# Kernel optimization log

Measured on AMD Instinct MI355X. Metric: run time of the kernel, lower is better.

The kernel has to match this reference:

```python
import jax, jax.numpy as jnp
import numpy as np

B, S, E, H = 2, 2048, 1024, 16
DH = E // H


def setup_inputs() -> dict:
    key = jax.random.key(0)
    ks = jax.random.split(key, 12)
    std = 1.0 / np.sqrt(E)
    inp = {
        "query": jax.random.normal(ks[0], (B, S, E), jnp.float32),
        "key": jax.random.normal(ks[1], (B, S, E), jnp.float32),
        "value": jax.random.normal(ks[2], (B, S, E), jnp.float32),
        "mask": jax.random.randint(ks[3], (B, 1, 1, S), 0, 2, jnp.int32),
        "Wq": jax.random.normal(ks[4], (E, E), jnp.float32) * std,
        "bq": jnp.zeros((E,), jnp.float32),
        "Wk": jax.random.normal(ks[5], (E, E), jnp.float32) * std,
        "bk": jnp.zeros((E,), jnp.float32),
        "Wv": jax.random.normal(ks[6], (E, E), jnp.float32) * std,
        "bv": jnp.zeros((E,), jnp.float32),
        "Wo": jax.random.normal(ks[7], (E, E), jnp.float32) * std,
        "bo": jnp.zeros((E,), jnp.float32),
    }
    return inp


def reference(query, key, value, mask, Wq, bq, Wk, bk, Wv, bv, Wo, bo):
    b = query.shape[0]
    # QKV projections, then split heads: [B,S,E] -> [B,H,S,Dh]
    def split_heads(x):
        return x.reshape(b, -1, H, DH).transpose(0, 2, 1, 3)
    q = split_heads(query @ Wq + bq)
    k = split_heads(key @ Wk + bk)
    v = split_heads(value @ Wv + bv)
    # explicit bmm -> mask -> softmax -> bmm (non-SDPA), scores [B,H,Sq,Sk]
    scores = jnp.einsum("bhqd,bhkd->bhqk", q, k) / np.sqrt(DH).astype(np.float32)
    scores = jnp.where(mask == 0, jnp.float32(-1e9), scores)
    attn = jax.nn.softmax(scores, axis=-1)  # dropout is identity in eval mode
    out = jnp.einsum("bhqk,bhkd->bhqd", attn, v)
    out = out.transpose(0, 2, 1, 3).reshape(b, -1, E)  # merge heads
    return out @ Wo + bo
```

## Files before the change

### kernel.cpp

```cpp
#include <hip/hip_runtime.h>
#include <hip/hip_bf16.h>
#include <stdint.h>

#define B_ 2
#define S_ 2048
#define E_ 1024
#define H_ 16
#define DH_ 64
#define MELEMS (4096 * 1024)
#define WE (1024 * 1024)

typedef unsigned short u16;
typedef __bf16 bf16x8 __attribute__((ext_vector_type(8)));
typedef u16 u16x8 __attribute__((ext_vector_type(8)));
typedef u16 u16x4 __attribute__((ext_vector_type(4)));
typedef float f32x4 __attribute__((ext_vector_type(4)));
typedef float f32x16 __attribute__((ext_vector_type(16)));
typedef uint32_t u32x4 __attribute__((ext_vector_type(4)));
typedef uint32_t u32x2v __attribute__((ext_vector_type(2)));

__device__ __forceinline__ float bf2f(u16 u) {
    union { uint32_t i; float f; } v; v.i = ((uint32_t)u) << 16; return v.f;
}
__device__ __forceinline__ u16 f2bf(float f) {
    union { float f; uint32_t i; } v; v.f = f;
    uint32_t r = (v.i + 0x7FFFu + ((v.i >> 16) & 1u)) >> 16;
    return (u16)r;
}
__device__ __forceinline__ uint32_t cvtpk(float a, float b) {
    uint32_t r;
    asm("v_cvt_pk_bf16_f32 %0, %1, %2" : "=v"(r) : "v"(a), "v"(b));
    return r;
}
__device__ __forceinline__ bf16x8 ldfrag(const u16* p) {
    u16x8 t = *(const u16x8*)p;
    return __builtin_bit_cast(bf16x8, t);
}
__device__ __forceinline__ void gld16(const void* g, void* l) {
    __builtin_amdgcn_global_load_lds(
        (const __attribute__((address_space(1))) void*)g,
        (__attribute__((address_space(3))) void*)l, 16, 0, 0);
}

__global__ __launch_bounds__(256)
void cvt_all(const float* __restrict__ q, const float* __restrict__ k,
             const float* __restrict__ v,
             const float* __restrict__ W0, const float* __restrict__ W1,
             const float* __restrict__ W2, const float* __restrict__ W3,
             u16* __restrict__ Qi, u16* __restrict__ Ki, u16* __restrict__ Vi,
             u16* __restrict__ T0, u16* __restrict__ T1,
             u16* __restrict__ T2, u16* __restrict__ T3)
{
    __shared__ float tile[64][65];
    const int bid = blockIdx.x;
    const int tid = threadIdx.x;

    if (bid < 6144) {
        const int z = bid >> 11;
        const int cx = bid & 2047;
        const float* src = (z == 0) ? q : (z == 1) ? k : v;
        u16* dst = (z == 0) ? Qi : (z == 1) ? Ki : Vi;
        const size_t i8 = ((size_t)cx * 256 + tid) * 8;
        float4 f0 = *(const float4*)&src[i8];
        float4 f1 = *(const float4*)&src[i8 + 4];
        u16x8 t;
        t[0] = f2bf(f0.x); t[1] = f2bf(f0.y); t[2] = f2bf(f0.z); t[3] = f2bf(f0.w);
        t[4] = f2bf(f1.x); t[5] = f2bf(f1.y); t[6] = f2bf(f1.z); t[7] = f2bf(f1.w);
        *(u16x8*)&dst[i8] = t;
    } else {
        const int rr = bid - 6144;
        const int z = rr >> 8;
        const int tt = rr & 255;
        const float* W = (z == 0) ? W0 : (z == 1) ? W1 : (z == 2) ? W2 : W3;
        u16* T = (z == 0) ? T0 : (z == 1) ? T1 : (z == 2) ? T2 : T3;
        const int n0 = (tt & 15) * 64, k0 = (tt >> 4) * 64;
        const int r = tid >> 2, c0 = (tid & 3) * 16;

        #pragma unroll
        for (int i = 0; i < 4; ++i) {
            float4 w = *(const float4*)&W[(size_t)(k0 + r) * 1024 + n0 + c0 + i * 4];
            tile[r][c0 + i * 4 + 0] = w.x; tile[r][c0 + i * 4 + 1] = w.y;
            tile[r][c0 + i * 4 + 2] = w.z; tile[r][c0 + i * 4 + 3] = w.w;
        }
        __syncthreads();
        u16x8 a, b;
        #pragma unroll
        for (int j = 0; j < 8; ++j) a[j] = f2bf(tile[c0 + j][r]);
        #pragma unroll
        for (int j = 0; j < 8; ++j) b[j] = f2bf(tile[c0 + 8 + j][r]);
        *(u16x8*)&T[(size_t)(n0 + r) * 1024 + k0 + c0] = a;
        *(u16x8*)&T[(size_t)(n0 + r) * 1024 + k0 + c0 + 8] = b;
    }
}

template<int BN>
__global__ __launch_bounds__(256)
void gemm_bt(const u16* __restrict__ A0, const u16* __restrict__ A1,
             const u16* __restrict__ A2,
             const u16* __restrict__ Bt0, const u16* __restrict__ Bt1,
             const u16* __restrict__ Bt2,
             const float* __restrict__ b0, const float* __restrict__ b1,
             const float* __restrict__ b2,
             void* __restrict__ C0, void* __restrict__ C1, void* __restrict__ C2,
             const int* __restrict__ mask,
             int c_f32, int vt_z, float scale0, int K)
{
    const int z = blockIdx.z;
    const u16* A  = (z == 0) ? A0 : (z == 1) ? A1 : A2;
    const u16* Bt = (z == 0) ? Bt0 : (z == 1) ? Bt1 : Bt2;
    const float* bias = (z == 0) ? b0 : (z == 1) ? b1 : b2;
    void* C = (z == 0) ? C0 : (z == 1) ? C1 : C2;
    const float scale = (z == 0) ? scale0 : 1.0f;

    __shared__ alignas(16) u16 As[128 * 32];
    __shared__ alignas(16) u16 Bs[BN * 32];

    const int tid  = threadIdx.x;
    const int lane = tid & 63;
    const int wv   = tid >> 6;
    const int l15  = lane & 15;
    const int quad = lane >> 4;
    const int m0 = blockIdx.y * 128;
    const int n0 = blockIdx.x * BN;
    const int wr = (wv >> 1) * 64;
    const int wc = (wv & 1) * (BN / 2);

    const int srow = wv * 16 + (lane >> 2);
    const int skk  = (lane & 3) * 8;

    constexpr int NJ = BN / 32;
    f32x4 acc[4][NJ] = {};

    for (int k0 = 0; k0 < K; k0 += 32) {
        __syncthreads();
        #pragma unroll
        for (int h = 0; h < 2; ++h) {
            const int r = h * 64 + srow;
            gld16(&A[(size_t)(m0 + r) * K + k0 + skk], &As[r * 32 + skk]);
        }
        #pragma unroll
        for (int h = 0; h < BN / 64; ++h) {
            const int r = h * 64 + srow;
            gld16(&Bt[(size_t)(n0 + r) * K + k0 + skk], &Bs[r * 32 + skk]);
        }
        __syncthreads();

        bf16x8 a[4], b[NJ];
        #pragma unroll
        for (int i = 0; i < 4; ++i)
            a[i] = ldfrag(&As[(wr + i * 16 + l15) * 32 + quad * 8]);
        #pragma unroll
        for (int j = 0; j < NJ; ++j)
            b[j] = ldfrag(&Bs[(wc + j * 16 + l15) * 32 + quad * 8]);
        #pragma unroll
        for (int i = 0; i < 4; ++i)
            #pragma unroll
            for (int j = 0; j < NJ; ++j)
                acc[i][j] = __builtin_amdgcn_mfma_f32_16x16x32_bf16(
                    a[i], b[j], acc[i][j], 0, 0, 0);
    }

    #pragma unroll
    for (int j = 0; j < NJ; ++j) {
        const int col = n0 + wc + j * 16 + l15;
        const float bcol = bias[col];
        #pragma unroll
        for (int i = 0; i < 4; ++i) {
            const int row0 = m0 + wr + i * 16 + quad * 4;
            if (z == vt_z) {
                const int bb = row0 >> 11, s0 = row0 & 2047;
                const int4 mv = *(const int4*)&mask[bb * S_ + s0];
                u16x4 t;
                t[0] = mv.x ? f2bf((acc[i][j][0] + bcol) * scale) : (u16)0;
                t[1] = mv.y ? f2bf((acc[i][j][1] + bcol) * scale) : (u16)0;
                t[2] = mv.z ? f2bf((acc[i][j][2] + bcol) * scale) : (u16)0;
                t[3] = mv.w ? f2bf((acc[i][j][3] + bcol) * scale) : (u16)0;
                *(u16x4*)&((u16*)C)[((size_t)bb * E_ + col) * S_ + s0] = t;
            } else {
                #pragma unroll
                for (int r = 0; r < 4; ++r) {
                    const int row = row0 + r;
                    const float v = (acc[i][j][r] + bcol) * scale;
                    if (c_f32) ((float*)C)[(size_t)row * 1024 + col] = v;
                    else       ((u16*)C)[(size_t)row * 1024 + col]  = f2bf(v);
                }
            }
        }
    }
}

__global__ __launch_bounds__(512, 4)
void attn_v12(const u16* __restrict__ Q, const u16* __restrict__ K,
              const u16* __restrict__ Vt_g, const int* __restrict__ mask,
              u16* __restrict__ ctx)
{
    __shared__ alignas(16) u16 smem[2][8192];
    __shared__ alignas(16) u16 Mbf[S_];
    __shared__ float scrl[256];

    const int tid  = threadIdx.x;
    const int lane = tid & 63;
    const int wv   = tid >> 6;
    const int l31  = lane & 31;
    const int half = lane >> 5;
    const int sw7  = lane & 7;
    const int qw   = wv & 3;
    const int kh   = wv >> 2;
    const int kbase = kh * 32;
    const int qt = blockIdx.x;
    const int bh = blockIdx.y;
    const int b  = bh >> 4, h = bh & 15;

    const size_t qk_off = (size_t)b * S_ * E_ + (size_t)h * DH_;
    const size_t vt_off = ((size_t)b * E_ + (size_t)h * DH_) * S_;
    const int* mrow = &mask[b * S_];

    {
        const int i = tid * 4;
        const int4 m = *(const int4*)&mrow[i];
        u16x4 t;
        t[0] = m.x ? (u16)0x3F80 : (u16)0;
        t[1] = m.y ? (u16)0x3F80 : (u16)0;
        t[2] = m.z ? (u16)0x3F80 : (u16)0;
        t[3] = m.w ? (u16)0x3F80 : (u16)0;
        *(u16x4*)&Mbf[i] = t;
    }

    const int q0 = qt * 128 + qw * 32;
    bf16x8 qf[4];
    #pragma unroll
    for (int s = 0; s < 4; ++s)
        qf[s] = ldfrag(&Q[qk_off + (size_t)(q0 + l31) * E_ + s * 16 + half * 8]);

    f32x16 O[2] = {};
    f32x16 lacc = {};

    auto stage = [&](int kc, int buf) {
        const int rr = tid >> 3;
        const int ks = tid & 7;
        const int gb = ks ^ (rr & 7);
        gld16(&K[qk_off + (size_t)(kc + rr) * E_ + gb * 8],
              &smem[buf][rr * 64 + ks * 8]);
        gld16(&Vt_g[vt_off + (size_t)rr * S_ + kc + gb * 8],
              &smem[buf][4096 + rr * 64 + ks * 8]);
    };

    stage(0, 0);
    int cur = 0;

    for (int kc = 0; kc < S_; kc += 64) {
        __syncthreads();
        if (kc + 64 < S_) stage(kc + 64, cur ^ 1);
        const u16* Kb = &smem[cur][0];
        const u16* Vb = &smem[cur][4096];

        __builtin_amdgcn_s_setprio(1);
        f32x16 St = {};
        #pragma unroll
        for (int s = 0; s < 4; ++s) {
            bf16x8 kf = ldfrag(&Kb[(kbase + l31) * 64 + ((s * 2 + half) ^ sw7) * 8]);
            St = __builtin_amdgcn_mfma_f32_32x32x16_bf16(kf, qf[s], St, 0, 0, 0);
        }
        __builtin_amdgcn_s_setprio(0);
        float ex[16];
        #pragma unroll
        for (int i = 0; i < 16; ++i) ex[i] = __builtin_exp2f(St[i]);

        uint32_t wd[8];
        #pragma unroll
        for (int i = 0; i < 8; ++i) wd[i] = cvtpk(ex[2 * i], ex[2 * i + 1]);

        u32x2v r02 = __builtin_amdgcn_permlane32_swap(wd[0], wd[2], false, false);
        u32x2v r13 = __builtin_amdgcn_permlane32_swap(wd[1], wd[3], false, false);
        u32x2v r46 = __builtin_amdgcn_permlane32_swap(wd[4], wd[6], false, false);
        u32x2v r57 = __builtin_amdgcn_permlane32_swap(wd[5], wd[7], false, false);
        u32x4 f0, f1;
        f0[0] = r02[0]; f0[1] = r13[0]; f0[2] = r02[1]; f0[3] = r13[1];
        f1[0] = r46[0]; f1[1] = r57[0]; f1[2] = r46[1]; f1[3] = r57[1];
        const bf16x8 pa0 = __builtin_bit_cast(bf16x8, f0);
        const bf16x8 pa1 = __builtin_bit_cast(bf16x8, f1);

        __builtin_amdgcn_s_setprio(1);
        {
            bf16x8 mb0 = ldfrag(&Mbf[kc + kbase + half * 8]);
            bf16x8 mb1 = ldfrag(&Mbf[kc + kbase + 16 + half * 8]);
            lacc = __builtin_amdgcn_mfma_f32_32x32x16_bf16(pa0, mb0, lacc, 0, 0, 0);
            lacc = __builtin_amdgcn_mfma_f32_32x32x16_bf16(pa1, mb1, lacc, 0, 0, 0);
        }

        #pragma unroll
        for (int nt = 0; nt < 2; ++nt) {
            const int drow = nt * 32 + l31;
            const int kb0 = kh * 4 + half;
            const int kb1 = kh * 4 + 2 + half;
            bf16x8 vb0 = ldfrag(&Vb[drow * 64 + (kb0 ^ sw7) * 8]);
            bf16x8 vb1 = ldfrag(&Vb[drow * 64 + (kb1 ^ sw7) * 8]);
            O[nt] = __builtin_amdgcn_mfma_f32_32x32x16_bf16(pa0, vb0, O[nt], 0, 0, 0);
            O[nt] = __builtin_amdgcn_mfma_f32_32x32x16_bf16(pa1, vb1, O[nt], 0, 0, 0);
        }
        __builtin_amdgcn_s_setprio(0);
        cur ^= 1;
    }

    __syncthreads();
    float* scr = (float*)smem;
    const int sbase = (qw * 64 + lane) * 32;
    if (kh == 1) {
        #pragma unroll
        for (int j = 0; j < 4; ++j) {
            f32x4 t0, t1;
            #pragma unroll
            for (int r = 0; r < 4; ++r) { t0[r] = O[0][j * 4 + r]; t1[r] = O[1][j * 4 + r]; }
            *(f32x4*)&scr[sbase + (j ^ sw7) * 4]       = t0;
            *(f32x4*)&scr[sbase + ((j + 4) ^ sw7) * 4] = t1;
        }
        if (l31 == 0) {
            #pragma unroll
            for (int i = 0; i < 16; ++i)
                scrl[qw * 32 + half * 16 + i] = lacc[i];
        }
    }
    __syncthreads();
    if (kh == 0) {
        #pragma unroll
        for (int nt = 0; nt < 2; ++nt) {
            #pragma unroll
            for (int j = 0; j < 4; ++j) {
                const f32x4 p = *(const f32x4*)&scr[sbase + (((nt * 4 + j) ^ sw7)) * 4];
                #pragma unroll
                for (int r = 0; r < 4; ++r) {
                    const int i  = j * 4 + r;
                    const int ql = (i & 3) + 8 * (i >> 2) + 4 * half;
                    const float lt = lacc[i] + scrl[qw * 32 + half * 16 + i];
                    const float o  = O[nt][i] + p[r];
                    const int q = q0 + ql;
                    const int e = h * DH_ + nt * 32 + l31;
                    ctx[((size_t)b * S_ + q) * E_ + e] = f2bf(o / lt);
                }
            }
        }
    }
}

__global__ __launch_bounds__(256)
void gemm_bias(const void* __restrict__ A, int a_f32,
               const float* __restrict__ W, const float* __restrict__ bias,
               void* __restrict__ C, int c_f32,
               int M, int N, int K, float scale)
{
    __shared__ alignas(16) u16 As[64 * 32];
    __shared__ alignas(16) u16 Wt[64 * 32];
    const int tid  = threadIdx.x;
    const int lane = tid & 63;
    const int wv   = tid >> 6;
    const int l15  = lane & 15;
    const int quad = lane >> 4;
    const int m0 = blockIdx.y * 64, n0 = blockIdx.x * 64;
    const int wr = (wv >> 1) * 32, wc = (wv & 1) * 32;
    const int ar = tid >> 2, ac = (tid & 3) * 8;
    const int wk = tid >> 3, wn = (tid & 7) * 8;
    f32x4 acc[2][2] = {};
    for (int k0 = 0; k0 < K; k0 += 32) {
        __syncthreads();
        if (a_f32) {
            const float* Af = (const float*)A;
            const float* p = &Af[(size_t)(m0 + ar) * K + k0 + ac];
            float4 f0 = *(const float4*)p; float4 f1 = *(const float4*)(p + 4);
            u16x8 t;
            t[0] = f2bf(f0.x); t[1] = f2bf(f0.y); t[2] = f2bf(f0.z); t[3] = f2bf(f0.w);
            t[4] = f2bf(f1.x); t[5] = f2bf(f1.y); t[6] = f2bf(f1.z); t[7] = f2bf(f1.w);
            *(u16x8*)&As[ar * 32 + ac] = t;
        } else {
            const u16* Ab = (const u16*)A;
            *(u16x8*)&As[ar * 32 + ac] = *(const u16x8*)&Ab[(size_t)(m0 + ar) * K + k0 + ac];
        }
        {
            const float* p = &W[(size_t)(k0 + wk) * N + n0 + wn];
            float4 g0 = *(const float4*)p; float4 g1 = *(const float4*)(p + 4);
            float fv[8] = {g0.x, g0.y, g0.z, g0.w, g1.x, g1.y, g1.z, g1.w};
            #pragma unroll
            for (int j = 0; j < 8; ++j) Wt[(wn + j) * 32 + wk] = f2bf(fv[j]);
        }
        __syncthreads();
        bf16x8 a[2], b[2];
        #pragma unroll
        for (int sm = 0; sm < 2; ++sm) a[sm] = ldfrag(&As[(wr + sm * 16 + l15) * 32 + quad * 8]);
        #pragma unroll
        for (int sn = 0; sn < 2; ++sn) b[sn] = ldfrag(&Wt[(wc + sn * 16 + l15) * 32 + quad * 8]);
        #pragma unroll
        for (int sm = 0; sm < 2; ++sm)
            #pragma unroll
            for (int sn = 0; sn < 2; ++sn)
                acc[sm][sn] = __builtin_amdgcn_mfma_f32_16x16x32_bf16(a[sm], b[sn], acc[sm][sn], 0, 0, 0);
    }
    #pragma unroll
    for (int sm = 0; sm < 2; ++sm)
        #pragma unroll
        for (int sn = 0; sn < 2; ++sn) {
            const int col = n0 + wc + sn * 16 + l15;
            const float bcol = bias[col];
            #pragma unroll
            for (int r = 0; r < 4; ++r) {
                const int row = m0 + wr + sm * 16 + quad * 4 + r;
                const float v = (acc[sm][sn][r] + bcol) * scale;
                if (c_f32) ((float*)C)[(size_t)row * N + col] = v;
                else       ((u16*)C)[(size_t)row * N + col]  = f2bf(v);
            }
        }
}

__global__ __launch_bounds__(256)
void attn_v2(const u16* __restrict__ Q, const u16* __restrict__ K,
             const u16* __restrict__ V, const int* __restrict__ mask,
             u16* __restrict__ ctx, int BH_per_B)
{
    __shared__ alignas(16) u16 Ks[64 * 72];
    __shared__ alignas(16) u16 Vt[64 * 72];
    __shared__ alignas(16) u16 Pb[4][16 * 72];
    const int tid  = threadIdx.x;
    const int lane = tid & 63;
    const int wv   = tid >> 6;
    const int l15  = lane & 15;
    const int quad = lane >> 4;
    const int qt = blockIdx.x;
    const int bh = blockIdx.y;
    const int b  = bh / BH_per_B, h = bh % BH_per_B;
    const size_t headoff = (size_t)b * S_ * E_ + (size_t)h * DH_;
    const int qrow = qt * 64 + wv * 16 + l15;
    const bf16x8 qf0 = ldfrag(&Q[headoff + (size_t)qrow * E_ + quad * 8]);
    const bf16x8 qf1 = ldfrag(&Q[headoff + (size_t)qrow * E_ + 32 + quad * 8]);
    f32x4 oacc[4] = {};
    float mrun[4] = {-1e30f, -1e30f, -1e30f, -1e30f};
    float lrun[4] = {0.f, 0.f, 0.f, 0.f};
    const int skey = tid >> 2;
    const int sd0  = (tid & 3) * 16;
    for (int kc = 0; kc < S_; kc += 64) {
        __syncthreads();
        {
            const u16* kg = &K[headoff + (size_t)(kc + skey) * E_ + sd0];
            *(u16x8*)&Ks[skey * 72 + sd0]     = *(const u16x8*)kg;
            *(u16x8*)&Ks[skey * 72 + sd0 + 8] = *(const u16x8*)(kg + 8);
            const u16* vg = &V[headoff + (size_t)(kc + skey) * E_ + sd0];
            u16x8 v0 = *(const u16x8*)vg;
            u16x8 v1 = *(const u16x8*)(vg + 8);
            #pragma unroll
            for (int j = 0; j < 8; ++j) {
                const int d = sd0 + j;
                Vt[d * 72 + (skey ^ (((d >> 3) & 7) * 8))] = v0[j];
            }
            #pragma unroll
            for (int j = 0; j < 8; ++j) {
                const int d = sd0 + 8 + j;
                Vt[d * 72 + (skey ^ (((d >> 3) & 7) * 8))] = v1[j];
            }
        }
        __syncthreads();
        f32x4 sb[4];
        #pragma unroll
        for (int t = 0; t < 4; ++t) {
            bf16x8 kf0 = ldfrag(&Ks[(t * 16 + l15) * 72 + quad * 8]);
            bf16x8 kf1 = ldfrag(&Ks[(t * 16 + l15) * 72 + 32 + quad * 8]);
            f32x4 s = {};
            s = __builtin_amdgcn_mfma_f32_16x16x32_bf16(qf0, kf0, s, 0, 0, 0);
            s = __builtin_amdgcn_mfma_f32_16x16x32_bf16(qf1, kf1, s, 0, 0, 0);
            const int mv = mask[b * S_ + kc + t * 16 + l15];
            #pragma unroll
            for (int r = 0; r < 4; ++r) sb[t][r] = (mv == 0) ? -1e9f : s[r];
        }
        #pragma unroll
        for (int r = 0; r < 4; ++r) {
            float m = fmaxf(fmaxf(sb[0][r], sb[1][r]), fmaxf(sb[2][r], sb[3][r]));
            #pragma unroll
            for (int off = 1; off < 16; off <<= 1) m = fmaxf(m, __shfl_xor(m, off));
            const float mnew  = fmaxf(mrun[r], m);
            const float alpha = __expf(mrun[r] - mnew);
            mrun[r] = mnew;
            float sum = 0.f;
            #pragma unroll
            for (int t = 0; t < 4; ++t) {
                const float p = __expf(sb[t][r] - mnew);
                sb[t][r] = p; sum += p;
            }
            #pragma unroll
            for (int off = 1; off < 16; off <<= 1) sum += __shfl_xor(sum, off);
            lrun[r] = lrun[r] * alpha + sum;
            #pragma unroll
            for (int c = 0; c < 4; ++c) oacc[c][r] *= alpha;
        }
        #pragma unroll
        for (int t = 0; t < 4; ++t)
            #pragma unroll
            for (int r = 0; r < 4; ++r)
                Pb[wv][(quad * 4 + r) * 72 + t * 16 + l15] = f2bf(sb[t][r]);
        const bf16x8 pa0 = ldfrag(&Pb[wv][l15 * 72 + quad * 8]);
        const bf16x8 pa1 = ldfrag(&Pb[wv][l15 * 72 + 32 + quad * 8]);
        #pragma unroll
        for (int c = 0; c < 4; ++c) {
            const int d = c * 16 + l15;
            const int sg = ((d >> 3) & 7) * 8;
            bf16x8 vb0 = ldfrag(&Vt[d * 72 + ((quad * 8) ^ sg)]);
            bf16x8 vb1 = ldfrag(&Vt[d * 72 + ((32 + quad * 8) ^ sg)]);
            oacc[c] = __builtin_amdgcn_mfma_f32_16x16x32_bf16(pa0, vb0, oacc[c], 0, 0, 0);
            oacc[c] = __builtin_amdgcn_mfma_f32_16x16x32_bf16(pa1, vb1, oacc[c], 0, 0, 0);
        }
    }
    #pragma unroll
    for (int c = 0; c < 4; ++c) {
        const int e = h * DH_ + c * 16 + l15;
        #pragma unroll
        for (int r = 0; r < 4; ++r) {
            const int qg = qt * 64 + wv * 16 + quad * 4 + r;
            ctx[((size_t)b * S_ + qg) * E_ + e] = f2bf(oacc[c][r] / lrun[r]);
        }
    }
}

extern "C" void kernel_launch(void* const* d_in, const int* in_sizes, int n_in,
                              void* d_out, int out_size, void* d_ws, size_t ws_size,
                              hipStream_t stream)
{
    const float* query = (const float*)d_in[0];
    const float* key   = (const float*)d_in[1];
    const float* value = (const float*)d_in[2];
    const int*   mask  = (const int*)d_in[3];
    const float* Wq = (const float*)d_in[4];  const float* bq = (const float*)d_in[5];
    const float* Wk = (const float*)d_in[6];  const float* bk = (const float*)d_in[7];
    const float* Wv = (const float*)d_in[8];  const float* bv = (const float*)d_in[9];
    const float* Wo = (const float*)d_in[10]; const float* bo = (const float*)d_in[11];
    float* out = (float*)d_out;

    u16* ws = (u16*)d_ws;
    dim3 blk(256);

    const size_t need_fancy = (size_t)(6 * MELEMS + 4 * WE) * sizeof(u16);
    const size_t need_full  = (size_t)(4 * MELEMS) * sizeof(u16) + 64;

    if (ws_size >= need_fancy) {
        u16* Qi  = ws;
        u16* Ki  = Qi + MELEMS;
        u16* Vi  = Ki + MELEMS;
        u16* Wqt = Vi + MELEMS;
        u16* Wkt = Wqt + WE;
        u16* Wvt = Wkt + WE;
        u16* Wot = Wvt + WE;
        u16* Qp  = Wot + WE;
        u16* Kp  = Qp + MELEMS;
        u16* Vp  = Kp + MELEMS;
        u16* Cp  = Qi;

        cvt_all<<<dim3(7168), blk, 0, stream>>>(query, key, value,
                                                Wq, Wk, Wv, Wo,
                                                Qi, Ki, Vi, Wqt, Wkt, Wvt, Wot);

        gemm_bt<128><<<dim3(8, 32, 3), blk, 0, stream>>>(
            Qi, Ki, Vi, Wqt, Wkt, Wvt, bq, bk, bv,
            Qp, Kp, Vp, mask, 0, 2, 0.125f * 1.44269504f, E_);

        attn_v12<<<dim3(S_ / 128, B_ * H_), dim3(512), 0, stream>>>(
            Qp, Kp, Vp, mask, Cp);

        gemm_bt<64><<<dim3(16, 32, 1), blk, 0, stream>>>(
            Cp, Cp, Cp, Wot, Wot, Wot, bo, bo, bo,
            out, out, out, mask, 1, -1, 1.0f, E_);
    } else if (ws_size >= need_full) {
        u16* Qp = ws;
        u16* Kp = ws + MELEMS;
        u16* Vp = ws + 2 * MELEMS;
        u16* Cp = ws + 3 * MELEMS;
        const int M = B_ * S_;
        dim3 gg(E_ / 64, M / 64);
        gemm_bias<<<gg, blk, 0, stream>>>(query, 1, Wq, bq, Qp, 0, M, E_, E_, 0.125f);
        gemm_bias<<<gg, blk, 0, stream>>>(key,   1, Wk, bk, Kp, 0, M, E_, E_, 1.0f);
        gemm_bias<<<gg, blk, 0, stream>>>(value, 1, Wv, bv, Vp, 0, M, E_, E_, 1.0f);
        attn_v2<<<dim3(S_ / 64, B_ * H_), blk, 0, stream>>>(Qp, Kp, Vp, mask, Cp, H_);
        gemm_bias<<<gg, blk, 0, stream>>>(Cp, 0, Wo, bo, out, 1, M, E_, E_, 1.0f);
    } else {
        const size_t szb = (size_t)S_ * E_;
        u16* Qp = ws; u16* Kp = ws + szb; u16* Vp = ws + 2 * szb; u16* Cp = ws + 3 * szb;
        dim3 gg(E_ / 64, S_ / 64);
        for (int b = 0; b < B_; ++b) {
            gemm_bias<<<gg, blk, 0, stream>>>(query + b * szb, 1, Wq, bq, Qp, 0, S_, E_, E_, 0.125f);
            gemm_bias<<<gg, blk, 0, stream>>>(key   + b * szb, 1, Wk, bk, Kp, 0, S_, E_, E_, 1.0f);
            gemm_bias<<<gg, blk, 0, stream>>>(value + b * szb, 1, Wv, bv, Vp, 0, S_, E_, E_, 1.0f);
            attn_v2<<<dim3(S_ / 64, H_), blk, 0, stream>>>(Qp, Kp, Vp, mask + b * S_, Cp, H_);
            gemm_bias<<<gg, blk, 0, stream>>>(Cp, 0, Wo, bo, ((float*)d_out) + b * szb, 1, S_, E_, E_, 1.0f);
        }
    }
}
```

Before: 149.8 us.

## Split attention over two key halves with fp32 partials and combine kernel

```diff
diff --git a/kernel.cpp b/kernel.cpp
--- a/kernel.cpp
+++ b/kernel.cpp
@@ -187,6 +187,188 @@
             }
         }
     }
+}
+
+__global__ __launch_bounds__(512, 4)
+void attn_v13(const u16* __restrict__ Q, const u16* __restrict__ K,
+              const u16* __restrict__ Vt_g, const int* __restrict__ mask,
+              float* __restrict__ Op0, float* __restrict__ Op1,
+              float* __restrict__ lp0, float* __restrict__ lp1)
+{
+    __shared__ alignas(16) u16 smem[2][8192];
+    __shared__ alignas(16) u16 Mbf[S_];
+    __shared__ float scrl[256];
+
+    const int tid  = threadIdx.x;
+    const int lane = tid & 63;
+    const int wv   = tid >> 6;
+    const int l31  = lane & 31;
+    const int half = lane >> 5;
+    const int sw7  = lane & 7;
+    const int qw   = wv & 3;
+    const int kh   = wv >> 2;
+    const int kbase = kh * 32;
+    const int qt = blockIdx.x;
+    const int bh = blockIdx.y;
+    const int b  = bh >> 4, h = bh & 15;
+    const int ks = blockIdx.z;
+    float* Op = ks ? Op1 : Op0;
+    float* lp = ks ? lp1 : lp0;
+    const int kbeg = ks << 10, kend = kbeg + 1024;
+
+    const size_t qk_off = (size_t)b * S_ * E_ + (size_t)h * DH_;
+    const size_t vt_off = ((size_t)b * E_ + (size_t)h * DH_) * S_;
+    const int* mrow = &mask[b * S_];
+
+    {
+        const int i = tid * 4;
+        const int4 m = *(const int4*)&mrow[i];
+        u16x4 t;
+        t[0] = m.x ? (u16)0x3F80 : (u16)0;
+        t[1] = m.y ? (u16)0x3F80 : (u16)0;
+        t[2] = m.z ? (u16)0x3F80 : (u16)0;
+        t[3] = m.w ? (u16)0x3F80 : (u16)0;
+        *(u16x4*)&Mbf[i] = t;
+    }
+
+    const int q0 = qt * 128 + qw * 32;
+    bf16x8 qf[4];
+    #pragma unroll
+    for (int s = 0; s < 4; ++s)
+        qf[s] = ldfrag(&Q[qk_off + (size_t)(q0 + l31) * E_ + s * 16 + half * 8]);
+
+    f32x16 O[2] = {};
+    f32x16 lacc = {};
+
+    auto stage = [&](int kc, int buf) {
+        const int rr = tid >> 3;
+        const int ks2 = tid & 7;
+        const int gb = ks2 ^ (rr & 7);
+        gld16(&K[qk_off + (size_t)(kc + rr) * E_ + gb * 8],
+              &smem[buf][rr * 64 + ks2 * 8]);
+        gld16(&Vt_g[vt_off + (size_t)rr * S_ + kc + gb * 8],
+              &smem[buf][4096 + rr * 64 + ks2 * 8]);
+    };
+
+    stage(kbeg, 0);
+    int cur = 0;
+
+    for (int kc = kbeg; kc < kend; kc += 64) {
+        __syncthreads();
+        if (kc + 64 < kend) stage(kc + 64, cur ^ 1);
+        const u16* Kb = &smem[cur][0];
+        const u16* Vb = &smem[cur][4096];
+
+        __builtin_amdgcn_s_setprio(1);
+        f32x16 St = {};
+        #pragma unroll
+        for (int s = 0; s < 4; ++s) {
+            bf16x8 kf = ldfrag(&Kb[(kbase + l31) * 64 + ((s * 2 + half) ^ sw7) * 8]);
+            St = __builtin_amdgcn_mfma_f32_32x32x16_bf16(kf, qf[s], St, 0, 0, 0);
+        }
+        __builtin_amdgcn_s_setprio(0);
+        float ex[16];
+        #pragma unroll
+        for (int i = 0; i < 16; ++i) ex[i] = __builtin_exp2f(St[i]);
+
+        uint32_t wd[8];
+        #pragma unroll
+        for (int i = 0; i < 8; ++i) wd[i] = cvtpk(ex[2 * i], ex[2 * i + 1]);
+
+        u32x2v r02 = __builtin_amdgcn_permlane32_swap(wd[0], wd[2], false, false);
+        u32x2v r13 = __builtin_amdgcn_permlane32_swap(wd[1], wd[3], false, false);
+        u32x2v r46 = __builtin_amdgcn_permlane32_swap(wd[4], wd[6], false, false);
+        u32x2v r57 = __builtin_amdgcn_permlane32_swap(wd[5], wd[7], false, false);
+        u32x4 f0, f1;
+        f0[0] = r02[0]; f0[1] = r13[0]; f0[2] = r02[1]; f0[3] = r13[1];
+        f1[0] = r46[0]; f1[1] = r57[0]; f1[2] = r46[1]; f1[3] = r57[1];
+        const bf16x8 pa0 = __builtin_bit_cast(bf16x8, f0);
+        const bf16x8 pa1 = __builtin_bit_cast(bf16x8, f1);
+
+        __builtin_amdgcn_s_setprio(1);
+        {
+            bf16x8 mb0 = ldfrag(&Mbf[kc + kbase + half * 8]);
+            bf16x8 mb1 = ldfrag(&Mbf[kc + kbase + 16 + half * 8]);
+            lacc = __builtin_amdgcn_mfma_f32_32x32x16_bf16(pa0, mb0, lacc, 0, 0, 0);
+            lacc = __builtin_amdgcn_mfma_f32_32x32x16_bf16(pa1, mb1, lacc, 0, 0, 0);
+        }
+
+        #pragma unroll
+        for (int nt = 0; nt < 2; ++nt) {
+            const int drow = nt * 32 + l31;
+            const int kb0 = kh * 4 + half;
+            const int kb1 = kh * 4 + 2 + half;
+            bf16x8 vb0 = ldfrag(&Vb[drow * 64 + (kb0 ^ sw7) * 8]);
+            bf16x8 vb1 = ldfrag(&Vb[drow * 64 + (kb1 ^ sw7) * 8]);
+            O[nt] = __builtin_amdgcn_mfma_f32_32x32x16_bf16(pa0, vb0, O[nt], 0, 0, 0);
+            O[nt] = __builtin_amdgcn_mfma_f32_32x32x16_bf16(pa1, vb1, O[nt], 0, 0, 0);
+        }
+        __builtin_amdgcn_s_setprio(0);
+        cur ^= 1;
+    }
+
+    __syncthreads();
+    float* scr = (float*)smem;
+    const int sbase = (qw * 64 + lane) * 32;
+    if (kh == 1) {
+        #pragma unroll
+        for (int j = 0; j < 4; ++j) {
+            f32x4 t0, t1;
+            #pragma unroll
+            for (int r = 0; r < 4; ++r) { t0[r] = O[0][j * 4 + r]; t1[r] = O[1][j * 4 + r]; }
+            *(f32x4*)&scr[sbase + (j ^ sw7) * 4]       = t0;
+            *(f32x4*)&scr[sbase + ((j + 4) ^ sw7) * 4] = t1;
+        }
+        if (l31 == 0) {
+            #pragma unroll
+            for (int i = 0; i < 16; ++i)
+                scrl[qw * 32 + half * 16 + i] = lacc[i];
+        }
+    }
+    __syncthreads();
+    if (kh == 0) {
+        #pragma unroll
+        for (int nt = 0; nt < 2; ++nt) {
+            #pragma unroll
+            for (int j = 0; j < 4; ++j) {
+                const f32x4 p = *(const f32x4*)&scr[sbase + (((nt * 4 + j) ^ sw7)) * 4];
+                #pragma unroll
+                for (int r = 0; r < 4; ++r) {
+                    const int i  = j * 4 + r;
+                    const int ql = (i & 3) + 8 * (i >> 2) + 4 * half;
+                    const float lt = lacc[i] + scrl[qw * 32 + half * 16 + i];
+                    const float o  = O[nt][i] + p[r];
+                    const int q = q0 + ql;
+                    Op[((size_t)bh * S_ + q) * DH_ + nt * 32 + l31] = o;
+                    if (nt == 0 && l31 == 0) lp[(size_t)bh * S_ + q] = lt;
+                }
+            }
+        }
+    }
+}
+
+__global__ __launch_bounds__(256)
+void attn_combine(const float* __restrict__ Op0, const float* __restrict__ Op1,
+                  const float* __restrict__ lp0, const float* __restrict__ lp1,
+                  u16* __restrict__ ctx)
+{
+    const int gid = blockIdx.x * 256 + threadIdx.x;
+    const int dh0 = (gid & 7) * 8;
+    const int qg  = gid >> 3;
+    const float inv = 1.0f / (lp0[qg] + lp1[qg]);
+    const size_t base = (size_t)qg * DH_ + dh0;
+    const f32x4 a0 = *(const f32x4*)&Op0[base];
+    const f32x4 a1 = *(const f32x4*)&Op0[base + 4];
+    const f32x4 b0 = *(const f32x4*)&Op1[base];
+    const f32x4 b1 = *(const f32x4*)&Op1[base + 4];
+    u16x8 t;
+    #pragma unroll
+    for (int j = 0; j < 4; ++j) t[j]     = f2bf((a0[j] + b0[j]) * inv);
+    #pragma unroll
+    for (int j = 0; j < 4; ++j) t[4 + j] = f2bf((a1[j] + b1[j]) * inv);
+    const int bh = qg >> 11, q = qg & 2047;
+    const int b = bh >> 4, h = bh & 15;
+    *(u16x8*)&ctx[((size_t)b * S_ + q) * E_ + h * DH_ + dh0] = t;
 }
 
 __global__ __launch_bounds__(512, 4)
@@ -533,6 +715,7 @@
     dim3 blk(256);
 
     const size_t need_fancy = (size_t)(6 * MELEMS + 4 * WE) * sizeof(u16);
+    const size_t need_split = need_fancy + (size_t)MELEMS * sizeof(float);
     const size_t need_full  = (size_t)(4 * MELEMS) * sizeof(u16) + 64;
 
     if (ws_size >= need_fancy) {
@@ -556,8 +739,20 @@
             Qi, Ki, Vi, Wqt, Wkt, Wvt, bq, bk, bv,
             Qp, Kp, Vp, mask, 0, 2, 0.125f * 1.44269504f, E_);
 
-        attn_v12<<<dim3(S_ / 128, B_ * H_), dim3(512), 0, stream>>>(
-            Qp, Kp, Vp, mask, Cp);
+        if (ws_size >= need_split) {
+            float* Op0 = (float*)Ki;
+            float* lp0 = (float*)Wqt;
+            float* lp1 = (float*)Wkt;
+            float* Op1 = (float*)(Vp + MELEMS);
+
+            attn_v13<<<dim3(S_ / 128, B_ * H_, 2), dim3(512), 0, stream>>>(
+                Qp, Kp, Vp, mask, Op0, Op1, lp0, lp1);
+            attn_combine<<<dim3(MELEMS / 8 / 256), blk, 0, stream>>>(
+                Op0, Op1, lp0, lp1, Cp);
+        } else {
+            attn_v12<<<dim3(S_ / 128, B_ * H_), dim3(512), 0, stream>>>(
+                Qp, Kp, Vp, mask, Cp);
+        }
 
         gemm_bt<64><<<dim3(16, 32, 1), blk, 0, stream>>>(
             Cp, Cp, Cp, Wot, Wot, Wot, bo, bo, bo,
```

Result: slower. 159.7 us (+6.6%).
